# Performance work log

Hardware: AMD Instinct MI355X
Metric: run time of the kernel (lower is better)

## Reference

```python
import jax, jax.numpy as jnp
import numpy as np

CLIP_MIN = 0.0  # recurrent_clip_min resolved in build() when -1
CLIP_MAX = 1.0  # recurrent_clip_max default when timesteps unknown


def setup_inputs() -> dict:
    key = jax.random.key(0)
    k1, k2, k3 = jax.random.split(key, 3)
    B, T, D, U = 64, 512, 256, 512
    x = jax.random.normal(k1, (B, T, D), dtype=jnp.float32)
    h0 = jnp.zeros((B, U), dtype=jnp.float32)
    W = jax.random.normal(k2, (D, U), dtype=jnp.float32) * (1.0 / np.sqrt(D))
    u = jax.random.uniform(k3, (U,), dtype=jnp.float32)  # uniform in clip range
    b = jnp.zeros((U,), dtype=jnp.float32)
    return {"x": x, "h0": h0, "W": W, "u": u, "b": b}


def reference(x, h0, W, u, b):
    # IndRNN: h_t = relu(x_t @ W + h_{t-1} * u + b), u clipped to [0, 1]
    u_c = jnp.clip(u, CLIP_MIN, CLIP_MAX)
    # One-time input projection for all timesteps: [B,T,U]
    proj = jnp.einsum("btd,du->btu", x, W) + b
    proj_t = jnp.swapaxes(proj, 0, 1)  # [T,B,U] for scan over time

    def step(h, p_t):
        h_new = jax.nn.relu(p_t + h * u_c)
        return h_new, h_new

    _, hs = jax.lax.scan(step, h0, proj_t)  # hs: [T,B,U]
    return jnp.swapaxes(hs, 0, 1)  # [B,T,U]
```

## Files before the change

### kernel.cpp

```cpp
#include <hip/hip_runtime.h>


__device__ __forceinline__ unsigned short f2bf(float f) {
    unsigned int u = __float_as_uint(f);
    unsigned int r = (u + 0x7FFF + ((u >> 16) & 1)) >> 16;
    return (unsigned short)r;
}

typedef __bf16 bf16x8 __attribute__((ext_vector_type(8)));
typedef float f32x4 __attribute__((ext_vector_type(4)));

typedef const unsigned char __attribute__((address_space(1))) gc_t;
typedef unsigned char __attribute__((address_space(3))) lds_t;

__device__ __forceinline__ void gl_lds16(const void* g, void* l) {
    __builtin_amdgcn_global_load_lds((gc_t*)g, (lds_t*)l, 16, 0, 0);
}

__global__ __launch_bounds__(256) void conv_x(
    const float* __restrict__ x, unsigned short* __restrict__ xb, int n4)
{
    int i = blockIdx.x * blockDim.x + threadIdx.x;
    if (i >= n4) return;
    float4 v = *(const float4*)(x + (long)i * 4);
    ushort4 o;
    o.x = f2bf(v.x); o.y = f2bf(v.y); o.z = f2bf(v.z); o.w = f2bf(v.w);
    *(ushort4*)(xb + (long)i * 4) = o;
}

#define TC 64
#define GN 128

__global__ __launch_bounds__(256, 1) void indrnn_fused(
    const unsigned short* __restrict__ xb,
    const float* __restrict__ W,
    const float* __restrict__ bias,
    const float* __restrict__ h0,
    const float* __restrict__ uvec,
    float* __restrict__ out,
    int B, int T, int U)
{
    __shared__ char Xs[2][TC * 512];
    __shared__ char Ps[GN * TC * 4];

    const int tid  = threadIdx.x;
    const int lane = tid & 63;
    const int w    = tid >> 6;
    const int m    = lane & 15;
    const int quad = lane >> 4;
    const int b    = blockIdx.x;
    const int n0   = blockIdx.y * GN;
    const int tq   = (w >> 1) * 32;
    const int cq   = (w & 1) * 64;

    const unsigned short* xrow = xb + (long)b * T * 256;
    const int p  = lane & 31;
    const int hh = lane >> 5;

#pragma unroll
    for (int i = 0; i < 8; ++i) {
        int blk = i * 4 + w;
        int row = blk * 2 + hh;
        int gp  = p ^ (row & 15);
        gl_lds16(xrow + (long)row * 256 + gp * 8, &Xs[0][blk * 1024]);
    }

    bf16x8 bfr[4][8];
#pragma unroll
    for (int j = 0; j < 4; ++j)
#pragma unroll
        for (int kt = 0; kt < 8; ++kt) {
            const float* wp = W + (long)(kt * 32 + quad * 8) * U
                                + (n0 + cq + j * 16 + m);
            bf16x8 f;
#pragma unroll
            for (int e = 0; e < 8; ++e) f[e] = (__bf16)wp[(long)e * U];
            bfr[j][kt] = f;
        }

    float bb[4];
#pragma unroll
    for (int j = 0; j < 4; ++j) bb[j] = bias[n0 + cq + j * 16 + m];

    float uc = 0.0f, h = 0.0f;
    if (tid < GN) {
        uc = fminf(fmaxf(uvec[n0 + tid], 0.0f), 1.0f);
        h  = h0[(long)b * U + n0 + tid];
    }

    asm volatile("s_waitcnt vmcnt(0)" ::: "memory");
    __builtin_amdgcn_sched_barrier(0);
    __syncthreads();

    const int nch = T / TC;
    for (int c = 0; c < nch; ++c) {
        const int buf = c & 1;

        if (c + 1 < nch) {
            const unsigned short* gb = xrow + (long)(c + 1) * TC * 256;
#pragma unroll
            for (int i = 0; i < 8; ++i) {
                int blk = i * 4 + w;
                int row = blk * 2 + hh;
                int gp  = p ^ (row & 15);
                gl_lds16(gb + (long)row * 256 + gp * 8, &Xs[buf ^ 1][blk * 1024]);
            }
        }

        f32x4 acc[2][4];
#pragma unroll
        for (int i = 0; i < 2; ++i)
#pragma unroll
            for (int j = 0; j < 4; ++j) acc[i][j] = (f32x4){0.f, 0.f, 0.f, 0.f};

#pragma unroll
        for (int kt = 0; kt < 8; ++kt) {
            const int off = (((kt * 4 + quad) ^ m) * 16);
            bf16x8 a0 = *(const bf16x8*)(&Xs[buf][(tq + m) * 512 + off]);
            bf16x8 a1 = *(const bf16x8*)(&Xs[buf][(tq + 16 + m) * 512 + off]);
#pragma unroll
            for (int j = 0; j < 4; ++j) {
                acc[0][j] = __builtin_amdgcn_mfma_f32_16x16x32_bf16(
                    a0, bfr[j][kt], acc[0][j], 0, 0, 0);
                acc[1][j] = __builtin_amdgcn_mfma_f32_16x16x32_bf16(
                    a1, bfr[j][kt], acc[1][j], 0, 0, 0);
            }
        }

#pragma unroll
        for (int i = 0; i < 2; ++i)
#pragma unroll
            for (int j = 0; j < 4; ++j) {
                f32x4 v = acc[i][j];
                f32x4 vb = {v[0] + bb[j], v[1] + bb[j], v[2] + bb[j], v[3] + bb[j]};
                int col = cq + j * 16 + m;
                int g   = (tq >> 2) + i * 4 + quad;
                *(f32x4*)(Ps + col * 256 + (((g ^ (col & 7)) << 4))) = vb;
            }
        __syncthreads();

        if (tid < GN) {
            f32x4 pv[16];
            const int ub = tid * 256;
            const int ux = (tid & 7) << 4;
#pragma unroll
            for (int gg = 0; gg < 16; ++gg)
                pv[gg] = *(const f32x4*)(Ps + ub + ((gg << 4) ^ ux));
            float* og = out + ((long)b * T + c * TC) * U + n0 + tid;
#pragma unroll
            for (int gg = 0; gg < 16; ++gg)
#pragma unroll
                for (int e = 0; e < 4; ++e) {
                    h = fmaxf(fmaf(h, uc, pv[gg][e]), 0.0f);
                    og[(long)(gg * 4 + e) * U] = h;
                }
        }

        if (tid < GN) {
            asm volatile("s_waitcnt vmcnt(48)" ::: "memory");
        } else {
            asm volatile("s_waitcnt vmcnt(0)" ::: "memory");
        }
        __builtin_amdgcn_sched_barrier(0);
        __syncthreads();
    }
}

#define BM 128
#define BN 128
#define BK 8

__global__ __launch_bounds__(256) void indrnn_gemm_bias(
    const float* __restrict__ A, const float* __restrict__ Bm,
    const float* __restrict__ bias, float* __restrict__ C,
    int M, int N, int K)
{
    __shared__ float As[BK][BM];
    __shared__ float Bs[BK][BN];
    const int tid = threadIdx.x;
    const int row0 = blockIdx.x * BM, col0 = blockIdx.y * BN;
    const int tx = tid & 15, ty = tid >> 4;
    float acc[8][8];
#pragma unroll
    for (int i = 0; i < 8; ++i)
#pragma unroll
        for (int j = 0; j < 8; ++j) acc[i][j] = 0.0f;
    const int am = tid >> 1, ak = (tid & 1) * 4;
    const int bk = tid >> 5, bn = (tid & 31) * 4;
    const float* Aptr = A + (long)(row0 + am) * K + ak;
    const float* Bptr = Bm + (long)bk * N + col0 + bn;
    for (int kt = 0; kt < K; kt += BK) {
        float4 av = *(const float4*)(Aptr + kt);
        float4 bv = *(const float4*)(Bptr + (long)kt * N);
        As[ak + 0][am] = av.x; As[ak + 1][am] = av.y;
        As[ak + 2][am] = av.z; As[ak + 3][am] = av.w;
        *(float4*)&Bs[bk][bn] = bv;
        __syncthreads();
#pragma unroll
        for (int k = 0; k < BK; ++k) {
            float4 a0 = *(const float4*)&As[k][ty * 4];
            float4 a1 = *(const float4*)&As[k][64 + ty * 4];
            float4 b0 = *(const float4*)&Bs[k][tx * 4];
            float4 b1 = *(const float4*)&Bs[k][64 + tx * 4];
            float a[8] = {a0.x, a0.y, a0.z, a0.w, a1.x, a1.y, a1.z, a1.w};
            float bb2[8] = {b0.x, b0.y, b0.z, b0.w, b1.x, b1.y, b1.z, b1.w};
#pragma unroll
            for (int i = 0; i < 8; ++i)
#pragma unroll
                for (int j = 0; j < 8; ++j)
                    acc[i][j] = fmaf(a[i], bb2[j], acc[i][j]);
        }
        __syncthreads();
    }
    float bb[8];
#pragma unroll
    for (int j = 0; j < 4; ++j) {
        bb[j] = bias[col0 + tx * 4 + j];
        bb[j + 4] = bias[col0 + 64 + tx * 4 + j];
    }
#pragma unroll
    for (int i = 0; i < 8; ++i) {
        const int r = (i < 4) ? (ty * 4 + i) : (64 + ty * 4 + (i - 4));
        float* crow = C + (long)(row0 + r) * N + col0;
        float4 v0 = {acc[i][0] + bb[0], acc[i][1] + bb[1], acc[i][2] + bb[2], acc[i][3] + bb[3]};
        float4 v1 = {acc[i][4] + bb[4], acc[i][5] + bb[5], acc[i][6] + bb[6], acc[i][7] + bb[7]};
        *(float4*)(crow + tx * 4) = v0;
        *(float4*)(crow + 64 + tx * 4) = v1;
    }
}

#define SCAN_UNROLL 32

__global__ __launch_bounds__(256) void indrnn_scan(
    float* __restrict__ out, const float* __restrict__ h0,
    const float* __restrict__ u, int B, int T, int U)
{
    const int idx = blockIdx.x * blockDim.x + threadIdx.x;
    if (idx >= B * U) return;
    const int b = idx / U;
    const int un = idx - b * U;
    const float uc = fminf(fmaxf(u[un], 0.0f), 1.0f);
    float h = h0[(long)b * U + un];
    float* p = out + (long)b * T * U + un;
    for (int t = 0; t < T; t += SCAN_UNROLL) {
        float pv[SCAN_UNROLL];
#pragma unroll
        for (int i = 0; i < SCAN_UNROLL; ++i)
            pv[i] = p[(long)(t + i) * U];
#pragma unroll
        for (int i = 0; i < SCAN_UNROLL; ++i) {
            h = fmaxf(fmaf(h, uc, pv[i]), 0.0f);
            pv[i] = h;
        }
#pragma unroll
        for (int i = 0; i < SCAN_UNROLL; ++i)
            p[(long)(t + i) * U] = pv[i];
    }
}

extern "C" void kernel_launch(void* const* d_in, const int* in_sizes, int n_in,
                              void* d_out, int out_size, void* d_ws, size_t ws_size,
                              hipStream_t stream) {
    const float* x  = (const float*)d_in[0];
    const float* h0 = (const float*)d_in[1];
    const float* W  = (const float*)d_in[2];
    const float* u  = (const float*)d_in[3];
    const float* b  = (const float*)d_in[4];
    float* out = (float*)d_out;

    const int U = in_sizes[3];
    const int B = in_sizes[1] / U;
    const int D = in_sizes[2] / U;
    const int T = in_sizes[0] / (B * D);
    const int M = B * T;

    const size_t xb_bytes = (size_t)M * D * sizeof(unsigned short);
    const bool fused_ok = (D == 256) && (U % GN == 0) && (T % TC == 0) &&
                          (ws_size >= xb_bytes);

    if (fused_ok) {
        unsigned short* xb = (unsigned short*)d_ws;
        const int n4 = (M * D) / 4;
        conv_x<<<(n4 + 255) / 256, 256, 0, stream>>>(x, xb, n4);

        dim3 g(B, U / GN);
        indrnn_fused<<<g, 256, 0, stream>>>(xb, W, b, h0, u, out, B, T, U);
    } else {
        dim3 ggrid(M / BM, U / BN);
        indrnn_gemm_bias<<<ggrid, 256, 0, stream>>>(x, W, b, out, M, U, D);
        const int nthreads = B * U;
        indrnn_scan<<<(nthreads + 255) / 256, 256, 0, stream>>>(out, h0, u, B, T, U);
    }
}
```

Measured before the change: 117.2 us.

## Triple-buffer X chunks and delegate async loads to non-scan warps

Switches the X chunk staging from double to triple buffering, prefetching two chunks ahead. Only warps 2-3, which do not run the serial scan, issue the global-to-LDS loads, so the scan warps no longer carry outstanding loads or wait on them. The goal is to hide global load latency behind the scan phase and keep it off the critical path. In exchange LDS use grows by one 32KB buffer, the staging warps issue twice as many loads each, and the fused path now requires at least two chunks.

```diff
diff --git a/kernel.cpp b/kernel.cpp
--- a/kernel.cpp
+++ b/kernel.cpp
@@ -40,7 +40,7 @@
     float* __restrict__ out,
     int B, int T, int U)
 {
-    __shared__ char Xs[2][TC * 512];
+    __shared__ char Xs[3][TC * 512];
     __shared__ char Ps[GN * TC * 4];
 
     const int tid  = threadIdx.x;
@@ -52,18 +52,12 @@
     const int n0   = blockIdx.y * GN;
     const int tq   = (w >> 1) * 32;
     const int cq   = (w & 1) * 64;
+    const bool stager = (w >= 2);
 
     const unsigned short* xrow = xb + (long)b * T * 256;
     const int p  = lane & 31;
     const int hh = lane >> 5;
-
-#pragma unroll
-    for (int i = 0; i < 8; ++i) {
-        int blk = i * 4 + w;
-        int row = blk * 2 + hh;
-        int gp  = p ^ (row & 15);
-        gl_lds16(xrow + (long)row * 256 + gp * 8, &Xs[0][blk * 1024]);
-    }
+    const int nch = T / TC;
 
     bf16x8 bfr[4][8];
 #pragma unroll
@@ -88,22 +82,45 @@
         h  = h0[(long)b * U + n0 + tid];
     }
 
-    asm volatile("s_waitcnt vmcnt(0)" ::: "memory");
+    if (stager) {
+        const int w2 = w - 2;
+#pragma unroll
+        for (int i = 0; i < 16; ++i) {
+            int blk = w2 * 16 + i;
+            int row = blk * 2 + hh;
+            int gp  = p ^ (row & 15);
+            gl_lds16(xrow + (long)row * 256 + gp * 8, &Xs[0][blk * 1024]);
+        }
+        if (nch > 1) {
+            const unsigned short* g1 = xrow + (long)TC * 256;
+#pragma unroll
+            for (int i = 0; i < 16; ++i) {
+                int blk = w2 * 16 + i;
+                int row = blk * 2 + hh;
+                int gp  = p ^ (row & 15);
+                gl_lds16(g1 + (long)row * 256 + gp * 8, &Xs[1][blk * 1024]);
+            }
+            asm volatile("s_waitcnt vmcnt(16)" ::: "memory");
+        } else {
+            asm volatile("s_waitcnt vmcnt(0)" ::: "memory");
+        }
+    }
     __builtin_amdgcn_sched_barrier(0);
     __syncthreads();
 
-    const int nch = T / TC;
     for (int c = 0; c < nch; ++c) {
-        const int buf = c & 1;
-
-        if (c + 1 < nch) {
-            const unsigned short* gb = xrow + (long)(c + 1) * TC * 256;
-#pragma unroll
-            for (int i = 0; i < 8; ++i) {
-                int blk = i * 4 + w;
+        const int buf = c % 3;
+
+        if (stager && (c + 2 < nch)) {
+            const unsigned short* gb = xrow + (long)(c + 2) * TC * 256;
+            char* Xn = Xs[(c + 2) % 3];
+            const int w2 = w - 2;
+#pragma unroll
+            for (int i = 0; i < 16; ++i) {
+                int blk = w2 * 16 + i;
                 int row = blk * 2 + hh;
                 int gp  = p ^ (row & 15);
-                gl_lds16(gb + (long)row * 256 + gp * 8, &Xs[buf ^ 1][blk * 1024]);
+                gl_lds16(gb + (long)row * 256 + gp * 8, Xn + blk * 1024);
             }
         }
 
@@ -154,12 +171,12 @@
                     h = fmaxf(fmaf(h, uc, pv[gg][e]), 0.0f);
                     og[(long)(gg * 4 + e) * U] = h;
                 }
-        }
-
-        if (tid < GN) {
-            asm volatile("s_waitcnt vmcnt(48)" ::: "memory");
         } else {
-            asm volatile("s_waitcnt vmcnt(0)" ::: "memory");
+            if (c + 2 < nch) {
+                asm volatile("s_waitcnt vmcnt(16)" ::: "memory");
+            } else {
+                asm volatile("s_waitcnt vmcnt(0)" ::: "memory");
+            }
         }
         __builtin_amdgcn_sched_barrier(0);
         __syncthreads();
@@ -276,7 +293,7 @@
 
     const size_t xb_bytes = (size_t)M * D * sizeof(unsigned short);
     const bool fused_ok = (D == 256) && (U % GN == 0) && (T % TC == 0) &&
-                          (ws_size >= xb_bytes);
+                          (T / TC >= 2) && (ws_size >= xb_bytes);
 
     if (fused_ok) {
         unsigned short* xb = (unsigned short*)d_ws;
```

New measurement: 117.3 us. Within noise of the previous version (+0.1%).
